# Optimization experiments

Measured on AMD Instinct MI355X. Metric: run time of the kernel, lower is better.

The kernel has to match this reference:

```python
import jax, jax.numpy as jnp
import numpy as np

N_P, N_A, N_T = 20000, 10000, 5000
D_IN, D_OUT = 512, 256
E_P, E_A, E_T = 320000, 160000, 80000


def setup_inputs() -> dict:
    key = jax.random.key(0)
    ks = iter(jax.random.split(key, 64))

    def nrm(shape, scale=1.0):
        return jax.random.normal(next(ks), shape, dtype=jnp.float32) * scale

    def xav(shape):
        # xavier_uniform-like scale (gain 1.414), normal draw is fine for a baseline
        return nrm(shape, 1.414 * (2.0 / (shape[0] + shape[1])) ** 0.5)

    def edges(ne, n_src, n_dst):
        src = jax.random.randint(next(ks), (ne,), 0, n_src, dtype=jnp.int32)
        dst = jax.random.randint(next(ks), (ne,), 0, n_dst, dtype=jnp.int32)
        w = jax.random.uniform(next(ks), (ne,), dtype=jnp.float32) / 16.0  # ~normalized adj values
        return src, dst, w

    d = {}
    d["x_p"] = nrm((N_P, D_IN))
    d["x_a"] = nrm((N_A, D_IN))
    d["x_t"] = nrm((N_T, D_IN))
    d["e_p_a_src"], d["e_p_a_dst"], d["e_p_a_w"] = edges(E_P, N_A, N_P)
    d["e_p_t_src"], d["e_p_t_dst"], d["e_p_t_w"] = edges(E_P, N_T, N_P)
    d["e_a_p_src"], d["e_a_p_dst"], d["e_a_p_w"] = edges(E_A, N_P, N_A)
    d["e_a_t_src"], d["e_a_t_dst"], d["e_a_t_w"] = edges(E_A, N_T, N_A)
    d["e_t_p_src"], d["e_t_p_dst"], d["e_t_p_w"] = edges(E_T, N_P, N_T)
    d["e_t_a_src"], d["e_t_a_dst"], d["e_t_a_w"] = edges(E_T, N_A, N_T)
    # parameters for each target type k: W_proj per neighbor, w_self, w_share, w_att, w_cat, bias
    for k, nbs in (("p", ("a", "t")), ("a", ("p", "t")), ("t", ("p", "a"))):
        for nb in nbs:
            d[f"W_{k}_{nb}"] = xav((D_IN, D_OUT))
        d[f"ws_{k}"] = xav((D_IN, D_OUT))
        d[f"wsh_{k}"] = xav((D_OUT, D_OUT))
        d[f"watt_{k}"] = xav((2 * D_OUT, 1))
        d[f"wcat_{k}"] = xav((2 * D_OUT, D_OUT))
        d[f"b_{k}"] = xav((1, D_OUT))
    return d


def _hete_agg(x_self, w_self, w_share, w_att, w_cat, bias, nb_inputs):
    """nb_inputs: list of (x_nb, W_proj, src, dst, edge_w). Faithful to HeteAggregateLayer."""
    n = x_self.shape[0]
    self_ft = (x_self @ w_self) @ w_share  # [n, d]
    # per-relation: project -> spmm (gather + weighted segment-sum over dst) -> share
    nb_fts = [
        jax.ops.segment_sum((x_nb @ Wp)[src] * ew[:, None], dst, num_segments=n) @ w_share
        for (x_nb, Wp, src, dst, ew) in nb_inputs
    ]
    L = len(nb_fts)
    # e = leaky_relu(cat([cat(nb_ft,0), self_ft.repeat(L,1)],1) @ w_att)  -> [L*n, 1]
    e = jnp.concatenate(
        [jax.nn.leaky_relu(jnp.concatenate([f, self_ft], axis=1) @ w_att) for f in nb_fts],
        axis=0,
    )
    # NOTE: faithful replication of the original `e.view(-1, L)` reshape semantics
    att = jax.nn.softmax(e.reshape(n, L), axis=1)  # [n, L]
    agg = nb_fts[0] * att[:, 0:1]
    for i in range(1, L):
        agg = agg + nb_fts[i] * att[:, i : i + 1]
    return jnp.concatenate([agg, self_ft], axis=1) @ w_cat + bias


def reference(x_p, x_a, x_t,
              e_p_a_src, e_p_a_dst, e_p_a_w, e_p_t_src, e_p_t_dst, e_p_t_w,
              e_a_p_src, e_a_p_dst, e_a_p_w, e_a_t_src, e_a_t_dst, e_a_t_w,
              e_t_p_src, e_t_p_dst, e_t_p_w, e_t_a_src, e_t_a_dst, e_t_a_w,
              W_p_a, W_p_t, ws_p, wsh_p, watt_p, wcat_p, b_p,
              W_a_p, W_a_t, ws_a, wsh_a, watt_a, wcat_a, b_a,
              W_t_p, W_t_a, ws_t, wsh_t, watt_t, wcat_t, b_t):
    out_p = _hete_agg(x_p, ws_p, wsh_p, watt_p, wcat_p, b_p,
                      [(x_a, W_p_a, e_p_a_src, e_p_a_dst, e_p_a_w),
                       (x_t, W_p_t, e_p_t_src, e_p_t_dst, e_p_t_w)])
    out_a = _hete_agg(x_a, ws_a, wsh_a, watt_a, wcat_a, b_a,
                      [(x_p, W_a_p, e_a_p_src, e_a_p_dst, e_a_p_w),
                       (x_t, W_a_t, e_a_t_src, e_a_t_dst, e_a_t_w)])
    out_t = _hete_agg(x_t, ws_t, wsh_t, watt_t, wcat_t, b_t,
                      [(x_p, W_t_p, e_t_p_src, e_t_p_dst, e_t_p_w),
                       (x_a, W_t_a, e_t_a_src, e_t_a_dst, e_t_a_w)])
    return (out_p, out_a, out_t)
```

## Files before the change

### kernel.cpp

```cpp
#include <hip/hip_runtime.h>

namespace {

typedef short s16x8 __attribute__((ext_vector_type(8)));
typedef float f32x4 __attribute__((ext_vector_type(4)));

__device__ __forceinline__ float bf2f(unsigned short u) {
  return __uint_as_float(((unsigned)u) << 16);
}
__device__ __forceinline__ unsigned short f2bf(float f) {
  unsigned u = __float_as_uint(f);
  u += 0x7fffu + ((u >> 16) & 1u);
  return (unsigned short)(u >> 16);
}

typedef __attribute__((address_space(3))) unsigned int lds_u32;
typedef __attribute__((address_space(1))) const unsigned int glob_u32;
__device__ __forceinline__ void gl16(const void* g, void* l) {
  __builtin_amdgcn_global_load_lds((glob_u32*)g, (lds_u32*)l, 16, 0, 0);
}

__global__ __launch_bounds__(256) void cvt_x3(const float* __restrict__ x0,
                                              const float* __restrict__ x1,
                                              const float* __restrict__ x2,
                                              unsigned short* __restrict__ out) {
  size_t i = ((size_t)blockIdx.x * 256 + threadIdx.x) * 8;
  const float* src;
  size_t off;
  if (i < (size_t)20000 * 512) { src = x0; off = i; }
  else if (i < (size_t)30000 * 512) { src = x1; off = i - (size_t)20000 * 512; }
  else { src = x2; off = i - (size_t)30000 * 512; }
  float4 a = *(const float4*)(src + off);
  float4 b = *(const float4*)(src + off + 4);
  s16x8 v;
  v[0] = (short)f2bf(a.x); v[1] = (short)f2bf(a.y);
  v[2] = (short)f2bf(a.z); v[3] = (short)f2bf(a.w);
  v[4] = (short)f2bf(b.x); v[5] = (short)f2bf(b.y);
  v[6] = (short)f2bf(b.z); v[7] = (short)f2bf(b.w);
  *(s16x8*)(out + i) = v;
}

struct Tc6 { const float* src[6]; unsigned short* dst[6]; int R[6]; };
__global__ __launch_bounds__(256) void transpose_cvt(Tc6 a) {
  int mat = blockIdx.z;
  int R = a.R[mat];
  int r0 = blockIdx.y * 32, c0 = blockIdx.x * 32;
  if (r0 >= R) return;
  const float* __restrict__ src = a.src[mat];
  unsigned short* __restrict__ dst = a.dst[mat];
  __shared__ float T[32][33];
  int tx = threadIdx.x & 31, ty = threadIdx.x >> 5;
  #pragma unroll
  for (int j = 0; j < 4; ++j) {
    int r = ty + j * 8;
    T[r][tx] = src[(size_t)(r0 + r) * 256 + c0 + tx];
  }
  __syncthreads();
  #pragma unroll
  for (int j = 0; j < 4; ++j) {
    int c = ty + j * 8;
    dst[(size_t)(c0 + c) * R + r0 + tx] = f2bf(T[tx][c]);
  }
}

struct Comb9 { const unsigned short* A[9]; const float* B[9]; unsigned short* C[9]; };
__global__ __launch_bounds__(256) void combine_mfma(Comb9 g) {
  int z = blockIdx.z;
  const unsigned short* __restrict__ A = g.A[z];
  const float* __restrict__ B = g.B[z];
  unsigned short* __restrict__ C = g.C[z];
  int row0 = blockIdx.y * 128;
  int col0 = blockIdx.x * 128;
  __shared__ unsigned short As[128 * 40];
  __shared__ unsigned short Bs[128 * 40];
  int tid = threadIdx.x, lane = tid & 63, w = tid >> 6;
  int quad = lane >> 4, m16 = lane & 15;
  f32x4 acc[2][8];
  #pragma unroll
  for (int r = 0; r < 2; ++r)
    #pragma unroll
    for (int c = 0; c < 8; ++c) acc[r][c] = (f32x4){0.f, 0.f, 0.f, 0.f};
  for (int k0 = 0; k0 < 256; k0 += 32) {
    #pragma unroll
    for (int i = 0; i < 2; ++i) {
      int ch = tid + i * 256;
      int m = ch >> 2, kk = (ch & 3) * 8;
      *(s16x8*)&As[m * 40 + kk] = *(const s16x8*)(A + (size_t)(row0 + m) * 256 + k0 + kk);
      const float4* bp = (const float4*)(B + (size_t)(col0 + m) * 256 + k0 + kk);
      float4 b0 = bp[0], b1 = bp[1];
      s16x8 bv;
      bv[0] = (short)f2bf(b0.x); bv[1] = (short)f2bf(b0.y);
      bv[2] = (short)f2bf(b0.z); bv[3] = (short)f2bf(b0.w);
      bv[4] = (short)f2bf(b1.x); bv[5] = (short)f2bf(b1.y);
      bv[6] = (short)f2bf(b1.z); bv[7] = (short)f2bf(b1.w);
      *(s16x8*)&Bs[m * 40 + kk] = bv;
    }
    __syncthreads();
    s16x8 af[2], bf[8];
    #pragma unroll
    for (int r = 0; r < 2; ++r)
      af[r] = *(const s16x8*)&As[(w * 32 + r * 16 + m16) * 40 + quad * 8];
    #pragma unroll
    for (int c = 0; c < 8; ++c)
      bf[c] = *(const s16x8*)&Bs[(c * 16 + m16) * 40 + quad * 8];
    #pragma unroll
    for (int r = 0; r < 2; ++r)
      #pragma unroll
      for (int c = 0; c < 8; ++c)
        acc[r][c] = __builtin_amdgcn_mfma_f32_16x16x32_bf16(af[r], bf[c], acc[r][c], 0, 0, 0);
    __syncthreads();
  }
  #pragma unroll
  for (int r = 0; r < 2; ++r)
    #pragma unroll
    for (int i = 0; i < 4; ++i) {
      int row = row0 + w * 32 + r * 16 + quad * 4 + i;
      #pragma unroll
      for (int c = 0; c < 8; ++c)
        C[(size_t)row * 512 + col0 + c * 16 + m16] = f2bf(acc[r][c][i]);
    }
}

struct Proj9 { const unsigned short* A[9]; const unsigned short* Bt[9]; unsigned short* C[9]; int M[9]; };
__global__ __launch_bounds__(256) void proj_mfma9(Proj9 g) {
  int z = blockIdx.z;
  int M = g.M[z];
  int row0 = blockIdx.y * 128;
  if (row0 >= M) return;
  int col0 = blockIdx.x * 128;
  const unsigned short* __restrict__ A = g.A[z];
  const unsigned short* __restrict__ Bt = g.Bt[z];
  unsigned short* __restrict__ C = g.C[z];
  __shared__ unsigned short As[128 * 32];
  __shared__ unsigned short Bs[128 * 32];
  int tid = threadIdx.x, lane = tid & 63, w = tid >> 6;
  int quad = lane >> 4, m16 = lane & 15;
  int lr = lane >> 2, lk = (lane & 3) * 8;
  int r0g = row0 + w * 32 + lr;
  int r1g = r0g + 16;
  const unsigned short* a0p = A + (size_t)(r0g < M ? r0g : M - 1) * 512 + lk;
  const unsigned short* a1p = A + (size_t)(r1g < M ? r1g : M - 1) * 512 + lk;
  const unsigned short* b0p = Bt + (size_t)(col0 + w * 32 + lr) * 512 + lk;
  const unsigned short* b1p = b0p + (size_t)16 * 512;
  unsigned short* as0 = &As[w * 1024];
  unsigned short* as1 = &As[w * 1024 + 512];
  unsigned short* bs0 = &Bs[w * 1024];
  unsigned short* bs1 = &Bs[w * 1024 + 512];
  int wr = (w & 1) * 64, wc = (w >> 1) * 64;
  f32x4 acc[4][4];
  #pragma unroll
  for (int r = 0; r < 4; ++r)
    #pragma unroll
    for (int c = 0; c < 4; ++c) acc[r][c] = (f32x4){0.f, 0.f, 0.f, 0.f};
  for (int k0 = 0; k0 < 512; k0 += 32) {
    gl16(a0p + k0, as0);
    gl16(a1p + k0, as1);
    gl16(b0p + k0, bs0);
    gl16(b1p + k0, bs1);
    __syncthreads();
    s16x8 af[4], bf[4];
    #pragma unroll
    for (int r = 0; r < 4; ++r)
      af[r] = *(const s16x8*)&As[(wr + r * 16 + m16) * 32 + quad * 8];
    #pragma unroll
    for (int c = 0; c < 4; ++c)
      bf[c] = *(const s16x8*)&Bs[(wc + c * 16 + m16) * 32 + quad * 8];
    #pragma unroll
    for (int r = 0; r < 4; ++r)
      #pragma unroll
      for (int c = 0; c < 4; ++c)
        acc[r][c] = __builtin_amdgcn_mfma_f32_16x16x32_bf16(af[r], bf[c], acc[r][c], 0, 0, 0);
    __syncthreads();
  }
  #pragma unroll
  for (int r = 0; r < 4; ++r)
    #pragma unroll
    for (int i = 0; i < 4; ++i) {
      int row = row0 + wr + r * 16 + quad * 4 + i;
      if (row < M) {
        #pragma unroll
        for (int c = 0; c < 4; ++c)
          C[(size_t)row * 256 + col0 + wc + c * 16 + m16] = f2bf(acc[r][c][i]);
      }
    }
}

struct Edges6 { const int* src[6]; const int* dst[6]; const float* w[6]; int nE[6]; int cbase[6]; };

__global__ __launch_bounds__(256) void hist_all(Edges6 ep, int* __restrict__ counts) {
  int rho = blockIdx.y;
  int e = blockIdx.x * 256 + threadIdx.x;
  if (e >= ep.nE[rho]) return;
  atomicAdd(&counts[ep.cbase[rho] + ep.dst[rho][e]], 1);
}

__global__ __launch_bounds__(256) void scan1(const int* __restrict__ cnt, int* __restrict__ out,
                                             int* __restrict__ part, int len) {
  __shared__ int sh[256];
  int base = blockIdx.x * 2048 + threadIdx.x * 8;
  int v[8];
  int s = 0;
  #pragma unroll
  for (int j = 0; j < 8; ++j) {
    int i = base + j;
    int x = (i < len) ? cnt[i] : 0;
    v[j] = s;
    s += x;
  }
  sh[threadIdx.x] = s;
  __syncthreads();
  for (int off = 1; off < 256; off <<= 1) {
    int t = (threadIdx.x >= off) ? sh[threadIdx.x - off] : 0;
    __syncthreads();
    sh[threadIdx.x] += t;
    __syncthreads();
  }
  int texcl = sh[threadIdx.x] - s;
  #pragma unroll
  for (int j = 0; j < 8; ++j) {
    int i = base + j;
    if (i < len) out[i] = texcl + v[j];
  }
  if (threadIdx.x == 255) part[blockIdx.x] = sh[255];
}

__global__ void scan2(int* __restrict__ part, int nb, int* __restrict__ total_out) {
  __shared__ int sh[64];
  int t = threadIdx.x;
  int v = (t < nb) ? part[t] : 0;
  sh[t] = v;
  __syncthreads();
  for (int off = 1; off < 64; off <<= 1) {
    int x = (t >= off) ? sh[t - off] : 0;
    __syncthreads();
    sh[t] += x;
    __syncthreads();
  }
  if (t < nb) part[t] = sh[t] - v;
  if (t == 63) *total_out = sh[63];
}

__global__ __launch_bounds__(256) void scan3(int* __restrict__ offs, int* __restrict__ cursor,
                                             const int* __restrict__ part, int len) {
  int i = blockIdx.x * 256 + threadIdx.x;
  if (i >= len) return;
  int v = offs[i] + part[i >> 11];
  offs[i] = v;
  cursor[i] = v;
}

__global__ __launch_bounds__(256) void fill_all(Edges6 ep, int* __restrict__ cursor,
                                                unsigned int* __restrict__ pay) {
  int rho = blockIdx.y;
  int e = blockIdx.x * 256 + threadIdx.x;
  if (e >= ep.nE[rho]) return;
  int pos = atomicAdd(&cursor[ep.cbase[rho] + ep.dst[rho][e]], 1);
  pay[pos] = (((unsigned)f2bf(ep.w[rho][e])) << 16) | (unsigned)ep.src[rho][e];
}

struct Gather6 { const unsigned short* proj[6]; unsigned short* out[6]; int cb[6]; int n[6]; };
__global__ __launch_bounds__(256) void gather_all(Gather6 g, const int* __restrict__ offs,
                                                  const unsigned int* __restrict__ pay) {
  int rho = blockIdx.y;
  int n = g.n[rho];
  int d = blockIdx.x * 4 + (threadIdx.x >> 6);
  if (d >= n) return;
  int lane = threadIdx.x & 63, half = lane >> 5, l32 = lane & 31;
  const unsigned short* __restrict__ proj = g.proj[rho];
  const int* of = offs + g.cb[rho];
  int s0 = of[d], s1 = of[d + 1];
  float acc[8] = {};
  int e = s0 + half;
  for (; e + 2 < s1; e += 4) {
    unsigned int u0 = pay[e], u1 = pay[e + 2];
    float wt0 = bf2f((unsigned short)(u0 >> 16));
    float wt1 = bf2f((unsigned short)(u1 >> 16));
    s16x8 v0 = *(const s16x8*)(proj + (size_t)(u0 & 0xffffu) * 256 + l32 * 8);
    s16x8 v1 = *(const s16x8*)(proj + (size_t)(u1 & 0xffffu) * 256 + l32 * 8);
    #pragma unroll
    for (int j = 0; j < 8; ++j) {
      acc[j] = fmaf(bf2f((unsigned short)v0[j]), wt0, acc[j]);
      acc[j] = fmaf(bf2f((unsigned short)v1[j]), wt1, acc[j]);
    }
  }
  if (e < s1) {
    unsigned int u = pay[e];
    float wt = bf2f((unsigned short)(u >> 16));
    s16x8 v = *(const s16x8*)(proj + (size_t)(u & 0xffffu) * 256 + l32 * 8);
    #pragma unroll
    for (int j = 0; j < 8; ++j) acc[j] = fmaf(bf2f((unsigned short)v[j]), wt, acc[j]);
  }
  #pragma unroll
  for (int j = 0; j < 8; ++j) acc[j] += __shfl(acc[j], lane ^ 32, 64);
  if (half == 0) {
    s16x8 o;
    #pragma unroll
    for (int j = 0; j < 8; ++j) o[j] = (short)f2bf(acc[j]);
    *(s16x8*)(g.out[rho] + (size_t)d * 256 + l32 * 8) = o;
  }
}

struct Att3 { const unsigned short* nb[3]; const unsigned short* self[3];
              const float* watt[3]; float* att[3]; int n[3]; };
__global__ __launch_bounds__(256) void e_att3(Att3 g) {
  int z = blockIdx.z;
  int n = g.n[z];
  int wv = threadIdx.x >> 6;
  int idx = blockIdx.x * 4 + wv;
  int lane = threadIdx.x & 63;
  __shared__ float ev[4];
  float sum = 0.f;
  if (idx < 2 * n) {
    int i = idx < n ? idx : idx - n;
    ushort4 v  = *(const ushort4*)(g.nb[z] + (size_t)idx * 256 + (lane << 2));
    ushort4 sv = *(const ushort4*)(g.self[z] + (size_t)i * 256 + (lane << 2));
    float4 wa = *(const float4*)(g.watt[z] + (lane << 2));
    float4 wb = *(const float4*)(g.watt[z] + 256 + (lane << 2));
    sum = bf2f(v.x) * wa.x + bf2f(v.y) * wa.y + bf2f(v.z) * wa.z + bf2f(v.w) * wa.w +
          bf2f(sv.x) * wb.x + bf2f(sv.y) * wb.y + bf2f(sv.z) * wb.z + bf2f(sv.w) * wb.w;
    #pragma unroll
    for (int off = 32; off > 0; off >>= 1) sum += __shfl_down(sum, off, 64);
  }
  if (lane == 0) ev[wv] = sum;
  __syncthreads();
  if (threadIdx.x < 2) {
    int base = blockIdx.x * 4 + threadIdx.x * 2;
    if (base < 2 * n) {
      float f0 = ev[threadIdx.x * 2], f1 = ev[threadIdx.x * 2 + 1];
      f0 = f0 > 0.f ? f0 : 0.01f * f0;
      f1 = f1 > 0.f ? f1 : 0.01f * f1;
      float m = fmaxf(f0, f1);
      float a = expf(f0 - m), b = expf(f1 - m);
      float inv = 1.f / (a + b);
      g.att[z][base] = a * inv;
      g.att[z][base + 1] = b * inv;
    }
  }
}

struct Fin3 { const unsigned short* nb[3]; const unsigned short* self[3]; const float* att[3];
              const unsigned short* Wt[3]; const float* bias[3]; float* out[3]; int M[3]; };
__global__ __launch_bounds__(256, 3) void final_mfma3(Fin3 g) {
  int z = blockIdx.z;
  int M = g.M[z];
  int row0 = blockIdx.y * 64;
  if (row0 >= M) return;
  const unsigned short* __restrict__ nbft = g.nb[z];
  const unsigned short* __restrict__ selfb = g.self[z];
  const float* __restrict__ att = g.att[z];
  const unsigned short* __restrict__ Wt = g.Wt[z];
  __shared__ unsigned short As[64 * 40];
  __shared__ unsigned short Bs[256 * 40];
  int tid = threadIdx.x, lane = tid & 63, w = tid >> 6;
  int quad = lane >> 4, m16 = lane & 15;
  int am = tid >> 2, akk = (tid & 3) * 8;
  int gr = row0 + am;
  float a0 = 0.f, a1 = 0.f;
  if (gr < M) { a0 = att[2 * gr]; a1 = att[2 * gr + 1]; }
  f32x4 acc[4][4];
  #pragma unroll
  for (int r = 0; r < 4; ++r)
    #pragma unroll
    for (int c = 0; c < 4; ++c) acc[r][c] = (f32x4){0.f, 0.f, 0.f, 0.f};

  s16x8 pu0 = {}, pu1 = {};
  s16x8 pb[4];

  auto loadA = [&](int k0) {
    int kg = k0 + akk;
    if (gr < M) {
      if (kg < 256) {
        pu0 = *(const s16x8*)(nbft + (size_t)gr * 256 + kg);
        pu1 = *(const s16x8*)(nbft + ((size_t)M + gr) * 256 + kg);
      } else {
        pu0 = *(const s16x8*)(selfb + (size_t)gr * 256 + (kg - 256));
      }
    }
  };
  auto loadB = [&](int k0) {
    #pragma unroll
    for (int i = 0; i < 4; ++i) {
      int ch = tid + i * 256;
      int m = ch >> 2, kk = (ch & 3) * 8;
      pb[i] = *(const s16x8*)(Wt + (size_t)m * 512 + k0 + kk);
    }
  };
  auto storeLDS = [&](int k0) {
    int kg = k0 + akk;
    s16x8 v = {};
    if (gr < M) {
      if (kg < 256) {
        #pragma unroll
        for (int j = 0; j < 8; ++j)
          v[j] = (short)f2bf(fmaf(a0, bf2f((unsigned short)pu0[j]),
                                  a1 * bf2f((unsigned short)pu1[j])));
      } else {
        v = pu0;
      }
    }
    *(s16x8*)&As[am * 40 + akk] = v;
    #pragma unroll
    for (int i = 0; i < 4; ++i) {
      int ch = tid + i * 256;
      int m = ch >> 2, kk = (ch & 3) * 8;
      *(s16x8*)&Bs[m * 40 + kk] = pb[i];
    }
  };

  loadA(0); loadB(0); storeLDS(0);
  __syncthreads();
  for (int k0 = 0; k0 < 512; k0 += 32) {
    int kn = k0 + 32;
    if (kn < 512) { loadA(kn); loadB(kn); }
    s16x8 af[4], bf[4];
    #pragma unroll
    for (int r = 0; r < 4; ++r)
      af[r] = *(const s16x8*)&As[(r * 16 + m16) * 40 + quad * 8];
    #pragma unroll
    for (int c = 0; c < 4; ++c)
      bf[c] = *(const s16x8*)&Bs[(w * 64 + c * 16 + m16) * 40 + quad * 8];
    #pragma unroll
    for (int r = 0; r < 4; ++r)
      #pragma unroll
      for (int c = 0; c < 4; ++c)
        acc[r][c] = __builtin_amdgcn_mfma_f32_16x16x32_bf16(af[r], bf[c], acc[r][c], 0, 0, 0);
    __syncthreads();
    if (kn < 512) {
      storeLDS(kn);
      __syncthreads();
    }
  }
  const float* __restrict__ bias = g.bias[z];
  float* __restrict__ out = g.out[z];
  #pragma unroll
  for (int r = 0; r < 4; ++r)
    #pragma unroll
    for (int i = 0; i < 4; ++i) {
      int row = row0 + r * 16 + quad * 4 + i;
      if (row < M) {
        #pragma unroll
        for (int c = 0; c < 4; ++c) {
          int col = w * 64 + c * 16 + m16;
          out[(size_t)row * 256 + col] = acc[r][c][i] + bias[col];
        }
      }
    }
}

}

extern "C" void kernel_launch(void* const* d_in, const int* in_sizes, int n_in,
                              void* d_out, int out_size, void* d_ws, size_t ws_size,
                              hipStream_t stream) {
  (void)in_sizes; (void)n_in; (void)out_size; (void)ws_size;
  const float* x[3] = {(const float*)d_in[0], (const float*)d_in[1], (const float*)d_in[2]};

  char* p = (char*)d_ws;
  unsigned short* projfull = (unsigned short*)p;  p += (size_t)105000 * 256 * 2;
  unsigned short* nbft = (unsigned short*)p;      p += (size_t)70000 * 256 * 2;
  unsigned short* wcatbt = (unsigned short*)p;    p += (size_t)3 * 256 * 512 * 2;
  int* offs = (int*)p;                            p += (size_t)70004 * 4;
  int* counts = (int*)p;                          p += (size_t)70000 * 4;
  int* part = (int*)p;                            p += 256;
  float* att_buf = (float*)p;                     p += (size_t)70000 * 4;
  unsigned int* csr_pay = (unsigned int*)p;       p += (size_t)1120000 * 4;
  unsigned short* wshT = nbft;
  unsigned short* Wcbt = (unsigned short*)((char*)nbft + 393216);
  unsigned short* xb = (unsigned short*)d_out;

  const int n_of[3] = {20000, 10000, 5000};
  const int nbt[3][2] = {{1, 2}, {0, 2}, {0, 1}};
  const int ebase[3][2] = {{3, 6}, {9, 12}, {15, 18}};
  const int nE3[3] = {320000, 160000, 80000};
  const size_t out_off[3] = {0, (size_t)20000 * 256, (size_t)30000 * 256};
  const int tstart[3] = {0, 15000, 40000};
  const int selfoff[3] = {70000, 90000, 100000};
  const int nboff[3] = {0, 40000, 60000};
  const int xboff[3] = {0, 20000, 30000};

  cvt_x3<<<dim3(8750), 256, 0, stream>>>(x[0], x[1], x[2], xb);

  Tc6 tc;
  for (int t = 0; t < 3; ++t) {
    tc.src[t] = (const float*)d_in[21 + t * 7 + 3];
    tc.dst[t] = wshT + (size_t)t * 256 * 256;
    tc.R[t] = 256;
    tc.src[3 + t] = (const float*)d_in[21 + t * 7 + 5];
    tc.dst[3 + t] = wcatbt + (size_t)t * 256 * 512;
    tc.R[3 + t] = 512;
  }
  transpose_cvt<<<dim3(8, 16, 6), 256, 0, stream>>>(tc);

  Comb9 c9;
  for (int t = 0; t < 3; ++t) {
    int wb = 21 + t * 7;
    for (int j = 0; j < 3; ++j) {
      int combo = t * 3 + j;
      c9.A[combo] = wshT + (size_t)t * 256 * 256;
      c9.B[combo] = (const float*)d_in[wb + j];
      c9.C[combo] = Wcbt + (size_t)combo * 256 * 512;
    }
  }
  combine_mfma<<<dim3(4, 2, 9), 256, 0, stream>>>(c9);

  Edges6 ep;
  const int cbase[6] = {0, 20000, 40000, 50000, 60000, 65000};
  for (int t = 0; t < 3; ++t)
    for (int r = 0; r < 2; ++r) {
      int rho = t * 2 + r, eb = ebase[t][r];
      ep.src[rho] = (const int*)d_in[eb];
      ep.dst[rho] = (const int*)d_in[eb + 1];
      ep.w[rho] = (const float*)d_in[eb + 2];
      ep.nE[rho] = nE3[t];
      ep.cbase[rho] = cbase[rho];
    }
  hipMemsetAsync(counts, 0, (size_t)70000 * 4, stream);
  hist_all<<<dim3(1250, 6), 256, 0, stream>>>(ep, counts);
  scan1<<<35, 256, 0, stream>>>(counts, offs, part, 70000);
  scan2<<<1, 64, 0, stream>>>(part, 35, offs + 70000);
  scan3<<<274, 256, 0, stream>>>(offs, counts, part, 70000);
  fill_all<<<dim3(1250, 6), 256, 0, stream>>>(ep, counts, csr_pay);

  Proj9 pj;
  for (int t = 0; t < 3; ++t) {
    int nb0 = nbt[t][0], nb1 = nbt[t][1];
    int m0 = n_of[nb0];
    pj.A[t * 3 + 0] = xb + (size_t)xboff[nb0] * 512;
    pj.C[t * 3 + 0] = projfull + (size_t)tstart[t] * 256;
    pj.M[t * 3 + 0] = m0;
    pj.A[t * 3 + 1] = xb + (size_t)xboff[nb1] * 512;
    pj.C[t * 3 + 1] = projfull + (size_t)(tstart[t] + m0) * 256;
    pj.M[t * 3 + 1] = n_of[nb1];
    pj.A[t * 3 + 2] = xb + (size_t)xboff[t] * 512;
    pj.C[t * 3 + 2] = projfull + (size_t)selfoff[t] * 256;
    pj.M[t * 3 + 2] = n_of[t];
    for (int j = 0; j < 3; ++j)
      pj.Bt[t * 3 + j] = Wcbt + (size_t)(t * 3 + j) * 256 * 512;
  }
  proj_mfma9<<<dim3(2, 157, 9), 256, 0, stream>>>(pj);

  Gather6 gt;
  for (int t = 0; t < 3; ++t) {
    int m0 = n_of[nbt[t][0]];
    for (int r = 0; r < 2; ++r) {
      int rho = t * 2 + r;
      gt.proj[rho] = projfull + (size_t)(tstart[t] + (r ? m0 : 0)) * 256;
      gt.out[rho] = nbft + (size_t)(nboff[t] + r * n_of[t]) * 256;
      gt.cb[rho] = cbase[rho];
      gt.n[rho] = n_of[t];
    }
  }
  gather_all<<<dim3(5000, 6), 256, 0, stream>>>(gt, offs, csr_pay);

  Att3 at;
  for (int t = 0; t < 3; ++t) {
    at.nb[t] = nbft + (size_t)nboff[t] * 256;
    at.self[t] = projfull + (size_t)selfoff[t] * 256;
    at.watt[t] = (const float*)d_in[21 + t * 7 + 4];
    at.att[t] = att_buf + nboff[t];
    at.n[t] = n_of[t];
  }
  e_att3<<<dim3(10000, 1, 3), 256, 0, stream>>>(at);

  Fin3 fn;
  for (int t = 0; t < 3; ++t) {
    fn.nb[t] = nbft + (size_t)nboff[t] * 256;
    fn.self[t] = projfull + (size_t)selfoff[t] * 256;
    fn.att[t] = att_buf + nboff[t];
    fn.Wt[t] = wcatbt + (size_t)t * 256 * 512;
    fn.bias[t] = (const float*)d_in[21 + t * 7 + 6];
    fn.out[t] = (float*)d_out + out_off[t];
    fn.M[t] = n_of[t];
  }
  final_mfma3<<<dim3(1, 313, 3), 256, 0, stream>>>(fn);
}
```

Measured before the change: 485.5 us.

## Replace global-atomic CSR fill with coarse bucketing and LDS-local fine scatter

The histogram pass now also scatters packed (dst, weight, src) records into coarse buckets of 64 destinations, each split into 8 sub-cells. A per-bucket kernel then places the records into the CSR payload using shared-memory cursors, replacing the second pass over the edges that used global atomics. Cells that overflow go to a global overflow buffer, which every block scans. This adds a write and read of 8-byte records and reuses the projection buffer as scratch, and the overflow path could become costly if buckets are skewed.

```diff
diff --git a/kernel.cpp b/kernel.cpp
--- a/kernel.cpp
+++ b/kernel.cpp
@@ -187,11 +187,27 @@
 
 struct Edges6 { const int* src[6]; const int* dst[6]; const float* w[6]; int nE[6]; int cbase[6]; };
 
-__global__ __launch_bounds__(256) void hist_all(Edges6 ep, int* __restrict__ counts) {
+#define RSH 6
+#define NBUK 1094
+#define RCAP 224
+#define NOV 65536
+
+__global__ __launch_bounds__(256) void binscat(Edges6 ep, int* __restrict__ counts,
+                                               int* __restrict__ subcnt, int* __restrict__ ovcnt,
+                                               unsigned long long* __restrict__ rec,
+                                               unsigned long long* __restrict__ ovbuf) {
   int rho = blockIdx.y;
   int e = blockIdx.x * 256 + threadIdx.x;
   if (e >= ep.nE[rho]) return;
-  atomicAdd(&counts[ep.cbase[rho] + ep.dst[rho][e]], 1);
+  int sub = (blockIdx.y * gridDim.x + blockIdx.x) & 7;
+  int gd = ep.cbase[rho] + ep.dst[rho][e];
+  atomicAdd(&counts[gd], 1);
+  unsigned pay = (((unsigned)f2bf(ep.w[rho][e])) << 16) | (unsigned)ep.src[rho][e];
+  unsigned long long r = ((unsigned long long)(unsigned)gd << 32) | pay;
+  int cell = (gd >> RSH) * 8 + sub;
+  int pos = atomicAdd(&subcnt[cell], 1);
+  if (pos < RCAP) rec[(size_t)cell * RCAP + pos] = r;
+  else { int op = atomicAdd(ovcnt, 1); ovbuf[op & (NOV - 1)] = r; }
 }
 
 __global__ __launch_bounds__(256) void scan1(const int* __restrict__ cnt, int* __restrict__ out,
@@ -240,22 +256,50 @@
   if (t == 63) *total_out = sh[63];
 }
 
-__global__ __launch_bounds__(256) void scan3(int* __restrict__ offs, int* __restrict__ cursor,
+__global__ __launch_bounds__(256) void scan3(int* __restrict__ offs,
                                              const int* __restrict__ part, int len) {
   int i = blockIdx.x * 256 + threadIdx.x;
   if (i >= len) return;
-  int v = offs[i] + part[i >> 11];
-  offs[i] = v;
-  cursor[i] = v;
-}
-
-__global__ __launch_bounds__(256) void fill_all(Edges6 ep, int* __restrict__ cursor,
-                                                unsigned int* __restrict__ pay) {
-  int rho = blockIdx.y;
-  int e = blockIdx.x * 256 + threadIdx.x;
-  if (e >= ep.nE[rho]) return;
-  int pos = atomicAdd(&cursor[ep.cbase[rho] + ep.dst[rho][e]], 1);
-  pay[pos] = (((unsigned)f2bf(ep.w[rho][e])) << 16) | (unsigned)ep.src[rho][e];
+  offs[i] += part[i >> 11];
+}
+
+__global__ __launch_bounds__(256) void fine_fill(const int* __restrict__ offs,
+                                                 const int* __restrict__ subcnt,
+                                                 const unsigned long long* __restrict__ rec,
+                                                 const int* __restrict__ ovcnt,
+                                                 const unsigned long long* __restrict__ ovbuf,
+                                                 unsigned int* __restrict__ pay) {
+  int b = blockIdx.x;
+  __shared__ int cur[64];
+  int t = threadIdx.x;
+  if (t < 64) {
+    int gd = (b << RSH) + t;
+    cur[t] = (gd < 70000) ? offs[gd] : 0;
+  }
+  __syncthreads();
+  #pragma unroll 1
+  for (int s = 0; s < 8; ++s) {
+    int cell = b * 8 + s;
+    int cnt = subcnt[cell];
+    cnt = cnt < RCAP ? cnt : RCAP;
+    const unsigned long long* rp = rec + (size_t)cell * RCAP;
+    for (int i = t; i < cnt; i += 256) {
+      unsigned long long r = rp[i];
+      int ld = (int)(r >> 32) & 63;
+      int pos = atomicAdd(&cur[ld], 1);
+      pay[pos] = (unsigned)r;
+    }
+  }
+  int ovn = *ovcnt;
+  ovn = ovn < NOV ? ovn : NOV;
+  for (int i = t; i < ovn; i += 256) {
+    unsigned long long r = ovbuf[i];
+    int gd = (int)(r >> 32);
+    if ((gd >> RSH) == b) {
+      int pos = atomicAdd(&cur[gd & 63], 1);
+      pay[pos] = (unsigned)r;
+    }
+  }
 }
 
 struct Gather6 { const unsigned short* proj[6]; unsigned short* out[6]; int cb[6]; int n[6]; };
@@ -461,11 +505,15 @@
   unsigned short* wcatbt = (unsigned short*)p;    p += (size_t)3 * 256 * 512 * 2;
   int* offs = (int*)p;                            p += (size_t)70004 * 4;
   int* counts = (int*)p;                          p += (size_t)70000 * 4;
+  int* subcnt = (int*)p;                          p += (size_t)NBUK * 8 * 4;
+  int* ovcnt = (int*)p;                           p += 16;
   int* part = (int*)p;                            p += 256;
   float* att_buf = (float*)p;                     p += (size_t)70000 * 4;
   unsigned int* csr_pay = (unsigned int*)p;       p += (size_t)1120000 * 4;
   unsigned short* wshT = nbft;
   unsigned short* Wcbt = (unsigned short*)((char*)nbft + 393216);
+  unsigned long long* rec = (unsigned long long*)projfull;
+  unsigned long long* ovbuf = rec + (size_t)NBUK * 8 * RCAP;
   unsigned short* xb = (unsigned short*)d_out;
 
   const int n_of[3] = {20000, 10000, 5000};
@@ -514,12 +562,12 @@
       ep.nE[rho] = nE3[t];
       ep.cbase[rho] = cbase[rho];
     }
-  hipMemsetAsync(counts, 0, (size_t)70000 * 4, stream);
-  hist_all<<<dim3(1250, 6), 256, 0, stream>>>(ep, counts);
+  hipMemsetAsync(counts, 0, (size_t)70000 * 4 + (size_t)NBUK * 8 * 4 + 16, stream);
+  binscat<<<dim3(1250, 6), 256, 0, stream>>>(ep, counts, subcnt, ovcnt, rec, ovbuf);
   scan1<<<35, 256, 0, stream>>>(counts, offs, part, 70000);
   scan2<<<1, 64, 0, stream>>>(part, 35, offs + 70000);
-  scan3<<<274, 256, 0, stream>>>(offs, counts, part, 70000);
-  fill_all<<<dim3(1250, 6), 256, 0, stream>>>(ep, counts, csr_pay);
+  scan3<<<274, 256, 0, stream>>>(offs, part, 70000);
+  fine_fill<<<NBUK, 256, 0, stream>>>(offs, subcnt, rec, ovcnt, ovbuf, csr_pay);
 
   Proj9 pj;
   for (int t = 0; t < 3; ++t) {
```

New measurement: 547.3 us. 12.7% more time.

## Replace atomic CSR fill with two-pass bucketed binning through LDS staging

Applied to the files above, without the earlier changes.

The histogram and scatter-fill passes are replaced with a coarse binning kernel. It counts destinations, groups edges into 512-destination buckets via an LDS-staged local sort, and writes them contiguously into per-bucket buffers, with an overflow buffer as fallback. A second kernel then places records into the final CSR using LDS atomics per bucket instead of global atomics scattered across the whole array. This aims to cut random global atomic traffic and uncoalesced writes. The cost is an extra intermediate buffer aliased onto projfull and more complex code with capacity limits.

```diff
diff --git a/kernel.cpp b/kernel.cpp
--- a/kernel.cpp
+++ b/kernel.cpp
@@ -187,11 +187,86 @@
 
 struct Edges6 { const int* src[6]; const int* dst[6]; const float* w[6]; int nE[6]; int cbase[6]; };
 
-__global__ __launch_bounds__(256) void hist_all(Edges6 ep, int* __restrict__ counts) {
+#define BSH 9
+#define NB2 137
+#define CAP2 10240
+#define NOV 65536
+#define CH 4096
+#define NPAY 1120000
+
+__global__ __launch_bounds__(256) void bin1(Edges6 ep, int* __restrict__ counts,
+                                            int* __restrict__ bcur, int* __restrict__ ovcnt,
+                                            unsigned long long* __restrict__ rec2,
+                                            unsigned long long* __restrict__ ovbuf) {
   int rho = blockIdx.y;
-  int e = blockIdx.x * 256 + threadIdx.x;
-  if (e >= ep.nE[rho]) return;
-  atomicAdd(&counts[ep.cbase[rho] + ep.dst[rho][e]], 1);
+  int nE = ep.nE[rho];
+  int chunk = blockIdx.x * CH;
+  if (chunk >= nE) return;
+  int n = nE - chunk; if (n > CH) n = CH;
+  const int* __restrict__ srcp = ep.src[rho];
+  const int* __restrict__ dstp = ep.dst[rho];
+  const float* __restrict__ wp = ep.w[rho];
+  int cb = ep.cbase[rho];
+  __shared__ int h[256], excl[256], lcur[256], gbase[256];
+  __shared__ unsigned long long stage[CH];
+  int t = threadIdx.x;
+  h[t] = 0;
+  gbase[t] = 0;
+  __syncthreads();
+  int gd[16]; unsigned pv[16];
+  #pragma unroll
+  for (int j = 0; j < 16; ++j) {
+    int idx = t + j * 256;
+    gd[j] = -1;
+    if (idx < n) {
+      int e = chunk + idx;
+      int d = dstp[e];
+      int g = cb + d;
+      if (g < 0) g = 0;
+      if (g > 69999) g = 69999;
+      gd[j] = g;
+      pv[j] = (((unsigned)f2bf(wp[e])) << 16) | ((unsigned)srcp[e] & 0x7fffu);
+      atomicAdd(&counts[g], 1);
+      atomicAdd(&h[g >> BSH], 1);
+    }
+  }
+  __syncthreads();
+  int hv = h[t];
+  excl[t] = hv;
+  __syncthreads();
+  for (int off = 1; off < 256; off <<= 1) {
+    int v = (t >= off) ? excl[t - off] : 0;
+    __syncthreads();
+    excl[t] += v;
+    __syncthreads();
+  }
+  int ex = excl[t] - hv;
+  __syncthreads();
+  excl[t] = ex;
+  lcur[t] = ex;
+  if (t < NB2 && hv > 0) gbase[t] = atomicAdd(&bcur[t], hv);
+  __syncthreads();
+  #pragma unroll
+  for (int j = 0; j < 16; ++j) {
+    if (gd[j] >= 0) {
+      int b = gd[j] >> BSH;
+      int slot = atomicAdd(&lcur[b], 1);
+      if (slot >= 0 && slot < CH)
+        stage[slot] = ((unsigned long long)(unsigned)gd[j] << 32) | pv[j];
+    }
+  }
+  __syncthreads();
+  for (int s = t; s < n; s += 256) {
+    int lo = 0, hi = NB2 - 1;
+    while (lo < hi) {
+      int mid = (lo + hi + 1) >> 1;
+      if (excl[mid] <= s) lo = mid; else hi = mid - 1;
+    }
+    int b = lo;
+    int gp = gbase[b] + (s - excl[b]);
+    if (gp >= 0 && gp < CAP2) rec2[(size_t)b * CAP2 + gp] = stage[s];
+    else { int op = atomicAdd(ovcnt, 1); ovbuf[op & (NOV - 1)] = stage[s]; }
+  }
 }
 
 __global__ __launch_bounds__(256) void scan1(const int* __restrict__ cnt, int* __restrict__ out,
@@ -240,22 +315,46 @@
   if (t == 63) *total_out = sh[63];
 }
 
-__global__ __launch_bounds__(256) void scan3(int* __restrict__ offs, int* __restrict__ cursor,
+__global__ __launch_bounds__(256) void scan3(int* __restrict__ offs,
                                              const int* __restrict__ part, int len) {
   int i = blockIdx.x * 256 + threadIdx.x;
   if (i >= len) return;
-  int v = offs[i] + part[i >> 11];
-  offs[i] = v;
-  cursor[i] = v;
-}
-
-__global__ __launch_bounds__(256) void fill_all(Edges6 ep, int* __restrict__ cursor,
-                                                unsigned int* __restrict__ pay) {
-  int rho = blockIdx.y;
-  int e = blockIdx.x * 256 + threadIdx.x;
-  if (e >= ep.nE[rho]) return;
-  int pos = atomicAdd(&cursor[ep.cbase[rho] + ep.dst[rho][e]], 1);
-  pay[pos] = (((unsigned)f2bf(ep.w[rho][e])) << 16) | (unsigned)ep.src[rho][e];
+  offs[i] += part[i >> 11];
+}
+
+__global__ __launch_bounds__(512) void fine2(const int* __restrict__ offs,
+                                             const int* __restrict__ bcur,
+                                             const unsigned long long* __restrict__ rec2,
+                                             const int* __restrict__ ovcnt,
+                                             const unsigned long long* __restrict__ ovbuf,
+                                             unsigned int* __restrict__ pay) {
+  int b = blockIdx.x;
+  __shared__ int cur[512];
+  int t = threadIdx.x;
+  {
+    int gd = (b << BSH) + t;
+    cur[t] = (gd < 70000) ? offs[gd] : 0;
+  }
+  __syncthreads();
+  int nrec = bcur[b];
+  nrec = nrec < CAP2 ? nrec : CAP2;
+  const unsigned long long* rp = rec2 + (size_t)b * CAP2;
+  for (int i = t; i < nrec; i += 512) {
+    unsigned long long r = rp[i];
+    int ld = (int)(r >> 32) & 511;
+    int pos = atomicAdd(&cur[ld], 1);
+    if (pos >= 0 && pos < NPAY) pay[pos] = (unsigned)r;
+  }
+  int ovn = *ovcnt;
+  ovn = ovn < NOV ? ovn : NOV;
+  for (int i = t; i < ovn; i += 512) {
+    unsigned long long r = ovbuf[i];
+    int gd = (int)(r >> 32);
+    if ((gd >> BSH) == b) {
+      int pos = atomicAdd(&cur[gd & 511], 1);
+      if (pos >= 0 && pos < NPAY) pay[pos] = (unsigned)r;
+    }
+  }
 }
 
 struct Gather6 { const unsigned short* proj[6]; unsigned short* out[6]; int cb[6]; int n[6]; };
@@ -461,11 +560,15 @@
   unsigned short* wcatbt = (unsigned short*)p;    p += (size_t)3 * 256 * 512 * 2;
   int* offs = (int*)p;                            p += (size_t)70004 * 4;
   int* counts = (int*)p;                          p += (size_t)70000 * 4;
+  int* bcur = (int*)p;                            p += 160 * 4;
+  int* ovcnt = (int*)p;                           p += 16;
   int* part = (int*)p;                            p += 256;
   float* att_buf = (float*)p;                     p += (size_t)70000 * 4;
   unsigned int* csr_pay = (unsigned int*)p;       p += (size_t)1120000 * 4;
   unsigned short* wshT = nbft;
   unsigned short* Wcbt = (unsigned short*)((char*)nbft + 393216);
+  unsigned long long* rec2 = (unsigned long long*)projfull;
+  unsigned long long* ovbuf = rec2 + (size_t)NB2 * CAP2;
   unsigned short* xb = (unsigned short*)d_out;
 
   const int n_of[3] = {20000, 10000, 5000};
@@ -514,12 +617,12 @@
       ep.nE[rho] = nE3[t];
       ep.cbase[rho] = cbase[rho];
     }
-  hipMemsetAsync(counts, 0, (size_t)70000 * 4, stream);
-  hist_all<<<dim3(1250, 6), 256, 0, stream>>>(ep, counts);
+  hipMemsetAsync(counts, 0, (size_t)70000 * 4 + 160 * 4 + 16, stream);
+  bin1<<<dim3(79, 6), 256, 0, stream>>>(ep, counts, bcur, ovcnt, rec2, ovbuf);
   scan1<<<35, 256, 0, stream>>>(counts, offs, part, 70000);
   scan2<<<1, 64, 0, stream>>>(part, 35, offs + 70000);
-  scan3<<<274, 256, 0, stream>>>(offs, counts, part, 70000);
-  fill_all<<<dim3(1250, 6), 256, 0, stream>>>(ep, counts, csr_pay);
+  scan3<<<274, 256, 0, stream>>>(offs, part, 70000);
+  fine2<<<NB2, 512, 0, stream>>>(offs, bcur, rec2, ovcnt, ovbuf, csr_pay);
 
   Proj9 pj;
   for (int t = 0; t < 3; ++t) {
```

Result: faster. 445.6 us (-8.2%).
